# Performance work log

Hardware: AMD Instinct MI355X
Metric: run time of the kernel (lower is better)

Reference implementation:

```python
import jax, jax.numpy as jnp
import numpy as np

C = 256      # channels
G = 8        # groups
K = 9        # 3x3 sampling points (DCNv4 default kernel_size=3)
DWK = 3      # dw_kernel_size (wrapper passes kernel_size=3)
OFFSET_SCALE = 1.0
N, H, W = 8, 64, 64


def setup_inputs() -> dict:
    key = jax.random.key(0)
    ks = jax.random.split(key, 6)
    def init(k, shape, fan):
        return jax.random.normal(k, shape, jnp.float32) * (fan ** -0.5)
    return {
        "x": jax.random.normal(ks[0], (N, C, H, W), jnp.float32),
        "dw_w": init(ks[1], (C, 1, DWK, DWK), DWK * DWK),   # depthwise conv (OIHW, groups=C)
        "dw_b": jnp.zeros((C,), jnp.float32),
        "om_w": init(ks[2], (G * K * 3, C), C) * 0.01,       # offset/mask linear (small offsets)
        "om_b": jnp.zeros((G * K * 3,), jnp.float32),
        "vp_w": init(ks[3], (C, C), C),                      # value_proj
        "vp_b": jnp.zeros((C,), jnp.float32),
        "op_w": init(ks[4], (C, C), C),                      # output_proj (output_bias=False)
    }


def reference(x, dw_w, dw_b, om_w, om_b, vp_w, vp_b, op_w):
    n, c, h, w = x.shape
    cg = c // G
    L = h * w
    # b c h w -> b (h w) c
    xf = x.transpose(0, 2, 3, 1).reshape(n, L, c)
    value = (xf @ vp_w.T + vp_b).reshape(n, L, G, cg)
    # offset/mask branch: depthwise conv on raw input, then linear
    om_in = jax.lax.conv_general_dilated(
        x, dw_w, (1, 1), "SAME", feature_group_count=c,
        dimension_numbers=("NCHW", "OIHW", "NCHW")) + dw_b[None, :, None, None]
    om = om_in.transpose(0, 2, 3, 1).reshape(n, L, c) @ om_w.T + om_b  # (n, L, G*K*3)
    om = om.reshape(n, h, w, G, K * 3)
    off = om[..., : 2 * K].reshape(n, h, w, G, K, 2) * OFFSET_SCALE     # (dy, dx) per point
    mask = om[..., 2 * K:]                                              # (n,h,w,G,K) raw (DCNv4: no softmax)
    # base 3x3 dilation-1 grid centered at each pixel
    d = jnp.arange(-1, 2, dtype=jnp.float32)
    dy, dx = jnp.meshgrid(d, d, indexing="ij")
    base = jnp.stack([dy.ravel(), dx.ravel()], -1)  # (K, 2)
    py = (jnp.arange(h, dtype=jnp.float32).reshape(1, h, 1, 1, 1)
          + base[:, 0].reshape(1, 1, 1, 1, K) + off[..., 0])  # (n,h,w,G,K)
    px = (jnp.arange(w, dtype=jnp.float32).reshape(1, 1, w, 1, 1)
          + base[:, 1].reshape(1, 1, 1, 1, K) + off[..., 1])
    y0 = jnp.floor(py); x0 = jnp.floor(px)
    ty = py - y0; tx = px - x0
    y0i = y0.astype(jnp.int32); x0i = x0.astype(jnp.int32)

    def gather(yi, xi, wgt):
        valid = (yi >= 0) & (yi < h) & (xi >= 0) & (xi < w)
        idx = jnp.clip(yi, 0, h - 1) * w + jnp.clip(xi, 0, w - 1)       # (n,h,w,G,K)
        idx = idx.transpose(0, 1, 2, 4, 3).reshape(n, L * K, G)[..., None]
        g = jnp.take_along_axis(value, idx, axis=1)                     # (n, L*K, G, cg)
        g = g.reshape(n, h, w, K, G, cg).transpose(0, 1, 2, 4, 3, 5)    # (n,h,w,G,K,cg)
        return g * (wgt * valid)[..., None]

    sampled = (gather(y0i,     x0i,     (1 - ty) * (1 - tx))
             + gather(y0i,     x0i + 1, (1 - ty) * tx)
             + gather(y0i + 1, x0i,     ty * (1 - tx))
             + gather(y0i + 1, x0i + 1, ty * tx))
    out = jnp.einsum("nhwgk,nhwgkc->nhwgc", mask, sampled)  # mask-weighted aggregation
    out = out.reshape(n, L, c) @ op_w.T                      # output_proj (no bias)
    # b (h w) c -> b c h w
    return out.reshape(n, h, w, c).transpose(0, 3, 1, 2)
```

## Files before the change

### kernel.cpp

```cpp
#include <hip/hip_runtime.h>
#include <math.h>

#define N_  8
#define C_  256
#define G_  8
#define CG_ 32
#define K_  9
#define H_  64
#define W_  64
#define L_  (H_*W_)
#define OM_ 216
#define OMP_ 256

using frag_ab = __attribute__((ext_vector_type(8))) short;
using frag_cd = __attribute__((ext_vector_type(4))) float;

__device__ __forceinline__ unsigned short f2bf(float f) {
    unsigned int u = __float_as_uint(f);
    u += 0x7FFFu + ((u >> 16) & 1u);
    return (unsigned short)(u >> 16);
}
__device__ __forceinline__ float bflo(unsigned int u) { return __uint_as_float(u << 16); }
__device__ __forceinline__ float bfhi(unsigned int u) { return __uint_as_float(u & 0xFFFF0000u); }

__device__ __forceinline__ void gld16(const void* g, void* l) {
    __builtin_amdgcn_global_load_lds((const __attribute__((address_space(1))) void*)g,
                                     (__attribute__((address_space(3))) void*)l, 16, 0, 0);
}

__global__ __launch_bounds__(256) void prep_kernel(const float* __restrict__ x,
                                                   const float* __restrict__ w,
                                                   const float* __restrict__ b,
                                                   const float* __restrict__ vp_w,
                                                   const float* __restrict__ om_w,
                                                   const float* __restrict__ om_b,
                                                   const float* __restrict__ op_w,
                                                   unsigned short* __restrict__ xb,
                                                   unsigned short* __restrict__ omb,
                                                   unsigned short* __restrict__ vp_wb,
                                                   unsigned short* __restrict__ om_wb,
                                                   float* __restrict__ om_bp,
                                                   unsigned short* __restrict__ op_wb) {
    const int n = blockIdx.z, y = blockIdx.y, c0 = blockIdx.x * 32;
    const int tid = threadIdx.x;
    __shared__ float xs[3][32][66];
    __shared__ __align__(16) unsigned short os[2][64][40];
    if (tid < 192) {
        int r = tid / 64, c = (tid / 2) % 32, e = tid & 1;
        xs[r][c][e * 65] = 0.f;
    }
    const float* xbase = x + ((size_t)n * C_ + c0) * L_;
    for (int i = tid; i < 3 * 32 * 16; i += 256) {
        int r = i >> 9, rem = i & 511, c = rem >> 4, x4 = (rem & 15) * 4;
        int yy = y + r - 1;
        float4 v = make_float4(0.f, 0.f, 0.f, 0.f);
        if ((unsigned)yy < (unsigned)H_) v = *(const float4*)(xbase + (size_t)c * L_ + yy * W_ + x4);
        xs[r][c][1 + x4] = v.x; xs[r][c][2 + x4] = v.y;
        xs[r][c][3 + x4] = v.z; xs[r][c][4 + x4] = v.w;
    }
    __syncthreads();

    const int c = tid & 31, x0 = (tid >> 5) * 8;
    float wv[9];
#pragma unroll
    for (int i = 0; i < 9; i++) wv[i] = w[(c0 + c) * 9 + i];
    const float bias = b[c0 + c];
    float o[8];
#pragma unroll
    for (int j = 0; j < 8; j++) o[j] = bias;
#pragma unroll
    for (int r = 0; r < 3; r++) {
        float v[10];
#pragma unroll
        for (int d = 0; d < 10; d++) v[d] = xs[r][c][x0 + d];
#pragma unroll
        for (int j = 0; j < 8; j++)
            o[j] += wv[r * 3] * v[j] + wv[r * 3 + 1] * v[j + 1] + wv[r * 3 + 2] * v[j + 2];
    }
#pragma unroll
    for (int j = 0; j < 8; j++) {
        os[0][x0 + j][c] = f2bf(xs[1][c][1 + x0 + j]);
        os[1][x0 + j][c] = f2bf(o[j]);
    }
    __syncthreads();

    const int l = tid >> 2, c8 = (tid & 3) * 8;
    uint4 va = *(const uint4*)&os[0][l][c8];
    uint4 vc = *(const uint4*)&os[1][l][c8];
    size_t dst = ((size_t)n * L_ + y * W_ + l) * C_ + c0 + c8;
    *(uint4*)(xb + dst) = va;
    *(uint4*)(omb + dst) = vc;

    if (n == 0) {
        int idx = (blockIdx.x + 8 * blockIdx.y) * 256 + tid;
        if (idx < C_ * C_) {
            vp_wb[idx] = f2bf(vp_w[idx]);
            op_wb[idx] = f2bf(op_w[idx]);
            om_wb[idx] = (idx < OM_ * C_) ? f2bf(om_w[idx]) : (unsigned short)0;
        }
        if (idx < OMP_) om_bp[idx] = (idx < OM_) ? om_b[idx] : 0.f;
    }
}

__global__ __launch_bounds__(256) void gemm12_kernel(const unsigned short* __restrict__ xb,
                                                     const unsigned short* __restrict__ omb,
                                                     const unsigned short* __restrict__ vp_wb,
                                                     const unsigned short* __restrict__ om_wb,
                                                     const float* __restrict__ vp_b,
                                                     const float* __restrict__ om_bp,
                                                     unsigned short* __restrict__ valueb,
                                                     float* __restrict__ omf) {
    __shared__ unsigned short As[128 * 32];
    __shared__ unsigned short Bs[128 * 32];
    const int which = blockIdx.z;
    const unsigned short* A = which ? omb : xb;
    const unsigned short* B = which ? om_wb : vp_wb;
    const float* bias = which ? om_bp : vp_b;
    const int tid = threadIdx.x;
    const long i0 = (long)blockIdx.x * 128;
    const long j0 = (long)blockIdx.y * 128;
    const unsigned short* Ab = A + i0 * C_;
    const unsigned short* Bb = B + j0 * C_;
    const int wave = tid >> 6, lane = tid & 63;
    const int iw = (wave & 1) * 64, jw = (wave >> 1) * 64;
    const int lm = lane & 15, kq = lane >> 4;
    const int srow = tid >> 2, scol = (tid & 3) * 8;

    frag_cd acc[4][4];
#pragma unroll
    for (int a = 0; a < 4; a++)
#pragma unroll
        for (int c = 0; c < 4; c++) acc[a][c] = (frag_cd){0.f, 0.f, 0.f, 0.f};

    for (int k0 = 0; k0 < C_; k0 += 32) {
        const unsigned short* ga0 = Ab + (long)srow * C_ + k0 + scol;
        const unsigned short* gb0 = Bb + (long)srow * C_ + k0 + scol;
        gld16(ga0,            As + tid * 8);
        gld16(ga0 + 64 * C_,  As + 2048 + tid * 8);
        gld16(gb0,            Bs + tid * 8);
        gld16(gb0 + 64 * C_,  Bs + 2048 + tid * 8);
        __syncthreads();
        frag_ab af[4], bfr[4];
#pragma unroll
        for (int mi = 0; mi < 4; mi++)
            af[mi] = *(const frag_ab*)&As[(iw + mi * 16 + lm) * 32 + kq * 8];
#pragma unroll
        for (int ni = 0; ni < 4; ni++)
            bfr[ni] = *(const frag_ab*)&Bs[(jw + ni * 16 + lm) * 32 + kq * 8];
#pragma unroll
        for (int mi = 0; mi < 4; mi++)
#pragma unroll
            for (int ni = 0; ni < 4; ni++)
                acc[mi][ni] = __builtin_amdgcn_mfma_f32_16x16x32_bf16(af[mi], bfr[ni], acc[mi][ni], 0, 0, 0);
        __syncthreads();
    }

    float bv[4];
#pragma unroll
    for (int ni = 0; ni < 4; ni++)
        bv[ni] = bias[(int)(j0 + jw + ni * 16 + lm)];

    const long ibase = i0 + iw + kq * 4;
    const long jbase = j0 + jw + lm;
#pragma unroll
    for (int mi = 0; mi < 4; mi++) {
#pragma unroll
        for (int ni = 0; ni < 4; ni++) {
            long j = jbase + ni * 16;
#pragma unroll
            for (int r = 0; r < 4; r++) {
                long i = ibase + mi * 16 + r;
                float v = acc[mi][ni][r] + bv[ni];
                if (which)
                    omf[i * OMP_ + j] = v;
                else
                    valueb[i * C_ + j] = f2bf(v);
            }
        }
    }
}

__global__ __launch_bounds__(256) void gemm3_kernel(const unsigned short* __restrict__ A,
                                                    const unsigned short* __restrict__ B,
                                                    float* __restrict__ Dv) {
    __shared__ unsigned short As[128 * 32];
    __shared__ unsigned short Bs[128 * 32];
    const int tid = threadIdx.x;
    const long i0 = (long)blockIdx.x * 128;
    const long j0 = (long)blockIdx.y * 128;
    const unsigned short* Ab = A + i0 * C_;
    const unsigned short* Bb = B + (long)blockIdx.z * L_ * C_ + j0 * C_;
    const int wave = tid >> 6, lane = tid & 63;
    const int iw = (wave & 1) * 64, jw = (wave >> 1) * 64;
    const int lm = lane & 15, kq = lane >> 4;
    const int srow = tid >> 2, scol = (tid & 3) * 8;

    frag_cd acc[4][4];
#pragma unroll
    for (int a = 0; a < 4; a++)
#pragma unroll
        for (int c = 0; c < 4; c++) acc[a][c] = (frag_cd){0.f, 0.f, 0.f, 0.f};

    for (int k0 = 0; k0 < C_; k0 += 32) {
        const unsigned short* ga0 = Ab + (long)srow * C_ + k0 + scol;
        const unsigned short* gb0 = Bb + (long)srow * C_ + k0 + scol;
        gld16(ga0,            As + tid * 8);
        gld16(ga0 + 64 * C_,  As + 2048 + tid * 8);
        gld16(gb0,            Bs + tid * 8);
        gld16(gb0 + 64 * C_,  Bs + 2048 + tid * 8);
        __syncthreads();
        frag_ab af[4], bfr[4];
#pragma unroll
        for (int mi = 0; mi < 4; mi++)
            af[mi] = *(const frag_ab*)&As[(iw + mi * 16 + lm) * 32 + kq * 8];
#pragma unroll
        for (int ni = 0; ni < 4; ni++)
            bfr[ni] = *(const frag_ab*)&Bs[(jw + ni * 16 + lm) * 32 + kq * 8];
#pragma unroll
        for (int mi = 0; mi < 4; mi++)
#pragma unroll
            for (int ni = 0; ni < 4; ni++)
                acc[mi][ni] = __builtin_amdgcn_mfma_f32_16x16x32_bf16(af[mi], bfr[ni], acc[mi][ni], 0, 0, 0);
        __syncthreads();
    }

    float* Db = Dv + (long)blockIdx.z * C_ * L_;
    const long ibase = i0 + iw + kq * 4;
    const long jbase = j0 + jw + lm;
#pragma unroll
    for (int mi = 0; mi < 4; mi++) {
#pragma unroll
        for (int ni = 0; ni < 4; ni++) {
            long j = jbase + ni * 16;
#pragma unroll
            for (int r = 0; r < 4; r++) {
                long i = ibase + mi * 16 + r;
                Db[i * L_ + j] = acc[mi][ni][r];
            }
        }
    }
}

__global__ __launch_bounds__(256) void sample_kernel(const unsigned short* __restrict__ value,
                                                     const float* __restrict__ om,
                                                     unsigned short* __restrict__ interm) {
    const int n = blockIdx.y;
    const int l0 = blockIdx.x * 8;
    const int tid = threadIdx.x;

    __shared__ float sOm[8 * OM_];
    __shared__ float4 wgt[64][9];
    __shared__ uint4  soff[64][9];

    const float* omsrc = om + ((size_t)n * L_ + l0) * OMP_;
    for (int i = tid; i < 8 * OM_; i += 256) {
        int pp = i / OM_;
        sOm[i] = omsrc[pp * OMP_ + (i - pp * OM_)];
    }
    __syncthreads();

    for (int it = tid; it < 576; it += 256) {
        int pair = it / 9, k = it - pair * 9;
        int p = pair >> 3, g = pair & 7;
        int l = l0 + p, y = l >> 6, xp2 = l & 63;
        const float* so = &sOm[p * OM_ + g * 27];
        float offy = so[2 * k], offx = so[2 * k + 1], mk = so[18 + k];
        float py = (float)(y + k / 3 - 1) + offy;
        float px = (float)(xp2 + k % 3 - 1) + offx;
        float fy = floorf(py), fx = floorf(px);
        float ty = py - fy, tx = px - fx;
        int y0 = (int)fy, x0i = (int)fx;
        int y1 = y0 + 1, x1 = x0i + 1;
        float vy0 = ((unsigned)y0 < (unsigned)H_) ? 1.f : 0.f;
        float vy1 = ((unsigned)y1 < (unsigned)H_) ? 1.f : 0.f;
        float vx0 = ((unsigned)x0i < (unsigned)W_) ? 1.f : 0.f;
        float vx1 = ((unsigned)x1 < (unsigned)W_) ? 1.f : 0.f;
        int cy0 = min(max(y0, 0), H_ - 1), cy1 = min(max(y1, 0), H_ - 1);
        int cx0 = min(max(x0i, 0), W_ - 1), cx1 = min(max(x1, 0), W_ - 1);
        wgt[pair][k] = make_float4(mk * (1.f - ty) * (1.f - tx) * vy0 * vx0,
                                   mk * (1.f - ty) * tx         * vy0 * vx1,
                                   mk * ty         * (1.f - tx) * vy1 * vx0,
                                   mk * ty         * tx         * vy1 * vx1);
        soff[pair][k] = make_uint4((unsigned)((cy0 * W_ + cx0) << 9),
                                   (unsigned)((cy0 * W_ + cx1) << 9),
                                   (unsigned)((cy1 * W_ + cx0) << 9),
                                   (unsigned)((cy1 * W_ + cx1) << 9));
    }
    __syncthreads();

    const int pair = tid >> 2, p = pair >> 3, g = pair & 7, c8 = (tid & 3) * 8;
    const char* vb = (const char*)(value + (size_t)n * L_ * C_ + g * CG_ + c8);
    float acc[8] = {0.f, 0.f, 0.f, 0.f, 0.f, 0.f, 0.f, 0.f};
#pragma unroll
    for (int k = 0; k < K_; k++) {
        float4 wk = wgt[pair][k];
        uint4  ok = soff[pair][k];
        const uint4 v00 = *(const uint4*)(vb + ok.x);
        const uint4 v01 = *(const uint4*)(vb + ok.y);
        const uint4 v10 = *(const uint4*)(vb + ok.z);
        const uint4 v11 = *(const uint4*)(vb + ok.w);
#define ACC8(V, WW) { \
        acc[0] += WW * bflo(V.x); acc[1] += WW * bfhi(V.x); \
        acc[2] += WW * bflo(V.y); acc[3] += WW * bfhi(V.y); \
        acc[4] += WW * bflo(V.z); acc[5] += WW * bfhi(V.z); \
        acc[6] += WW * bflo(V.w); acc[7] += WW * bfhi(V.w); }
        ACC8(v00, wk.x) ACC8(v01, wk.y) ACC8(v10, wk.z) ACC8(v11, wk.w)
#undef ACC8
    }
    uint4 pk;
    unsigned short* pp2 = (unsigned short*)&pk;
#pragma unroll
    for (int i = 0; i < 8; i++) pp2[i] = f2bf(acc[i]);
    *(uint4*)(interm + ((size_t)n * L_ + l0 + p) * C_ + g * CG_ + c8) = pk;
}

extern "C" void kernel_launch(void* const* d_in, const int* in_sizes, int n_in,
                              void* d_out, int out_size, void* d_ws, size_t ws_size,
                              hipStream_t stream) {
    const float* x    = (const float*)d_in[0];
    const float* dw_w = (const float*)d_in[1];
    const float* dw_b = (const float*)d_in[2];
    const float* om_w = (const float*)d_in[3];
    const float* om_b = (const float*)d_in[4];
    const float* vp_w = (const float*)d_in[5];
    const float* vp_b = (const float*)d_in[6];
    const float* op_w = (const float*)d_in[7];
    float* out = (float*)d_out;

    char* ws = (char*)d_ws;
    unsigned short* xb      = (unsigned short*)(ws);
    unsigned short* omb     = (unsigned short*)(ws + 16777216);
    unsigned short* valueb  = (unsigned short*)(ws + 33554432);
    float*          omf     = (float*)(ws + 50331648);
    unsigned short* vp_wb   = (unsigned short*)(ws + 83886080);
    unsigned short* om_wb   = (unsigned short*)(ws + 84017152);
    unsigned short* op_wb   = (unsigned short*)(ws + 84148224);
    float*          om_bp   = (float*)(ws + 84279296);
    unsigned short* intermb = xb;

    prep_kernel<<<dim3(C_ / 32, H_, N_), 256, 0, stream>>>(
        x, dw_w, dw_b, vp_w, om_w, om_b, op_w,
        xb, omb, vp_wb, om_wb, om_bp, op_wb);
    gemm12_kernel<<<dim3(256, 2, 2), 256, 0, stream>>>(
        xb, omb, vp_wb, om_wb, vp_b, om_bp, valueb, omf);
    sample_kernel<<<dim3(L_ / 8, N_), 256, 0, stream>>>(valueb, omf, intermb);
    gemm3_kernel<<<dim3(2, 32, N_), 256, 0, stream>>>(op_wb, intermb, out);
}
```

Before: 174.4 us.

## Fuse deformable sampling with output projection GEMM via shared-memory intermediate

Merges the sampling kernel and the output-projection GEMM into one kernel. Each block samples 64 pixels across all groups into an XOR-swizzled LDS tile, then runs MFMA against op_w read straight from global memory. This removes the global write and re-read of the bf16 intermediate and one kernel launch. In exchange the sampling runs as 8 serialized sub-steps with barriers, there are fewer blocks (512), and op_w is reloaded from global/L2 by every block.

Result: faster. 168.7 us (-3.2%).

```diff
diff --git a/kernel.cpp b/kernel.cpp
--- a/kernel.cpp
+++ b/kernel.cpp
@@ -180,138 +180,120 @@
     }
 }
 
-__global__ __launch_bounds__(256) void gemm3_kernel(const unsigned short* __restrict__ A,
-                                                    const unsigned short* __restrict__ B,
-                                                    float* __restrict__ Dv) {
-    __shared__ unsigned short As[128 * 32];
-    __shared__ unsigned short Bs[128 * 32];
+__global__ __launch_bounds__(256, 3) void samplegemm_kernel(const unsigned short* __restrict__ value,
+                                                            const float* __restrict__ om,
+                                                            const unsigned short* __restrict__ opw,
+                                                            float* __restrict__ out) {
+    const int n = blockIdx.y, l0 = blockIdx.x * 64;
     const int tid = threadIdx.x;
-    const long i0 = (long)blockIdx.x * 128;
-    const long j0 = (long)blockIdx.y * 128;
-    const unsigned short* Ab = A + i0 * C_;
-    const unsigned short* Bb = B + (long)blockIdx.z * L_ * C_ + j0 * C_;
-    const int wave = tid >> 6, lane = tid & 63;
-    const int iw = (wave & 1) * 64, jw = (wave >> 1) * 64;
-    const int lm = lane & 15, kq = lane >> 4;
-    const int srow = tid >> 2, scol = (tid & 3) * 8;
-
-    frag_cd acc[4][4];
-#pragma unroll
-    for (int a = 0; a < 4; a++)
-#pragma unroll
-        for (int c = 0; c < 4; c++) acc[a][c] = (frag_cd){0.f, 0.f, 0.f, 0.f};
-
-    for (int k0 = 0; k0 < C_; k0 += 32) {
-        const unsigned short* ga0 = Ab + (long)srow * C_ + k0 + scol;
-        const unsigned short* gb0 = Bb + (long)srow * C_ + k0 + scol;
-        gld16(ga0,            As + tid * 8);
-        gld16(ga0 + 64 * C_,  As + 2048 + tid * 8);
-        gld16(gb0,            Bs + tid * 8);
-        gld16(gb0 + 64 * C_,  Bs + 2048 + tid * 8);
-        __syncthreads();
-        frag_ab af[4], bfr[4];
-#pragma unroll
-        for (int mi = 0; mi < 4; mi++)
-            af[mi] = *(const frag_ab*)&As[(iw + mi * 16 + lm) * 32 + kq * 8];
-#pragma unroll
-        for (int ni = 0; ni < 4; ni++)
-            bfr[ni] = *(const frag_ab*)&Bs[(jw + ni * 16 + lm) * 32 + kq * 8];
-#pragma unroll
-        for (int mi = 0; mi < 4; mi++)
-#pragma unroll
-            for (int ni = 0; ni < 4; ni++)
-                acc[mi][ni] = __builtin_amdgcn_mfma_f32_16x16x32_bf16(af[mi], bfr[ni], acc[mi][ni], 0, 0, 0);
-        __syncthreads();
-    }
-
-    float* Db = Dv + (long)blockIdx.z * C_ * L_;
-    const long ibase = i0 + iw + kq * 4;
-    const long jbase = j0 + jw + lm;
-#pragma unroll
-    for (int mi = 0; mi < 4; mi++) {
-#pragma unroll
-        for (int ni = 0; ni < 4; ni++) {
-            long j = jbase + ni * 16;
-#pragma unroll
-            for (int r = 0; r < 4; r++) {
-                long i = ibase + mi * 16 + r;
-                Db[i * L_ + j] = acc[mi][ni][r];
-            }
-        }
-    }
-}
-
-__global__ __launch_bounds__(256) void sample_kernel(const unsigned short* __restrict__ value,
-                                                     const float* __restrict__ om,
-                                                     unsigned short* __restrict__ interm) {
-    const int n = blockIdx.y;
-    const int l0 = blockIdx.x * 8;
-    const int tid = threadIdx.x;
-
-    __shared__ float sOm[8 * OM_];
+    __shared__ __align__(16) unsigned short interm[64 * 256];
     __shared__ float4 wgt[64][9];
     __shared__ uint4  soff[64][9];
 
-    const float* omsrc = om + ((size_t)n * L_ + l0) * OMP_;
-    for (int i = tid; i < 8 * OM_; i += 256) {
-        int pp = i / OM_;
-        sOm[i] = omsrc[pp * OMP_ + (i - pp * OM_)];
+    const char* vbase = (const char*)(value + (size_t)n * L_ * C_);
+    const int lp = tid >> 2;
+    const int g = lp & 7;
+    const int c8i = tid & 3;
+    const int slot = tid & 31;
+    const char* vb = vbase + (size_t)(g * CG_ + c8i * 8) * 2;
+
+    for (int rep = 0; rep < 8; rep++) {
+        __syncthreads();
+        for (int it = tid; it < 576; it += 256) {
+            int pl = it / 9, k = it - pl * 9;
+            int p = rep * 8 + (pl >> 3), gg = pl & 7;
+            int l = l0 + p, y = l >> 6, xp2 = l & 63;
+            const float* so = om + ((size_t)n * L_ + l) * OMP_ + gg * 27;
+            float offy = so[2 * k], offx = so[2 * k + 1], mk = so[18 + k];
+            float py = (float)(y + k / 3 - 1) + offy;
+            float px = (float)(xp2 + k % 3 - 1) + offx;
+            float fy = floorf(py), fx = floorf(px);
+            float ty = py - fy, tx = px - fx;
+            int y0 = (int)fy, x0i = (int)fx;
+            int y1 = y0 + 1, x1 = x0i + 1;
+            float vy0 = ((unsigned)y0 < (unsigned)H_) ? 1.f : 0.f;
+            float vy1 = ((unsigned)y1 < (unsigned)H_) ? 1.f : 0.f;
+            float vx0 = ((unsigned)x0i < (unsigned)W_) ? 1.f : 0.f;
+            float vx1 = ((unsigned)x1 < (unsigned)W_) ? 1.f : 0.f;
+            int cy0 = min(max(y0, 0), H_ - 1), cy1 = min(max(y1, 0), H_ - 1);
+            int cx0 = min(max(x0i, 0), W_ - 1), cx1 = min(max(x1, 0), W_ - 1);
+            wgt[pl][k] = make_float4(mk * (1.f - ty) * (1.f - tx) * vy0 * vx0,
+                                     mk * (1.f - ty) * tx         * vy0 * vx1,
+                                     mk * ty         * (1.f - tx) * vy1 * vx0,
+                                     mk * ty         * tx         * vy1 * vx1);
+            soff[pl][k] = make_uint4((unsigned)((cy0 * W_ + cx0) << 9),
+                                     (unsigned)((cy0 * W_ + cx1) << 9),
+                                     (unsigned)((cy1 * W_ + cx0) << 9),
+                                     (unsigned)((cy1 * W_ + cx1) << 9));
+        }
+        __syncthreads();
+        const int p = rep * 8 + (lp >> 3);
+        float acc[8] = {0.f, 0.f, 0.f, 0.f, 0.f, 0.f, 0.f, 0.f};
+#pragma unroll
+        for (int k = 0; k < K_; k++) {
+            float4 wk = wgt[lp][k];
+            uint4  ok = soff[lp][k];
+            const uint4 v00 = *(const uint4*)(vb + ok.x);
+            const uint4 v01 = *(const uint4*)(vb + ok.y);
+            const uint4 v10 = *(const uint4*)(vb + ok.z);
+            const uint4 v11 = *(const uint4*)(vb + ok.w);
+#define ACC8(V, WW) { \
+            acc[0] += WW * bflo(V.x); acc[1] += WW * bfhi(V.x); \
+            acc[2] += WW * bflo(V.y); acc[3] += WW * bfhi(V.y); \
+            acc[4] += WW * bflo(V.z); acc[5] += WW * bfhi(V.z); \
+            acc[6] += WW * bflo(V.w); acc[7] += WW * bfhi(V.w); }
+            ACC8(v00, wk.x) ACC8(v01, wk.y) ACC8(v10, wk.z) ACC8(v11, wk.w)
+#undef ACC8
+        }
+        uint4 pk;
+        unsigned short* ps = (unsigned short*)&pk;
+#pragma unroll
+        for (int i = 0; i < 8; i++) ps[i] = f2bf(acc[i]);
+        int phys = slot ^ (p & 7);
+        *(uint4*)&interm[p * 256 + phys * 8] = pk;
     }
     __syncthreads();
 
-    for (int it = tid; it < 576; it += 256) {
-        int pair = it / 9, k = it - pair * 9;
-        int p = pair >> 3, g = pair & 7;
-        int l = l0 + p, y = l >> 6, xp2 = l & 63;
-        const float* so = &sOm[p * OM_ + g * 27];
-        float offy = so[2 * k], offx = so[2 * k + 1], mk = so[18 + k];
-        float py = (float)(y + k / 3 - 1) + offy;
-        float px = (float)(xp2 + k % 3 - 1) + offx;
-        float fy = floorf(py), fx = floorf(px);
-        float ty = py - fy, tx = px - fx;
-        int y0 = (int)fy, x0i = (int)fx;
-        int y1 = y0 + 1, x1 = x0i + 1;
-        float vy0 = ((unsigned)y0 < (unsigned)H_) ? 1.f : 0.f;
-        float vy1 = ((unsigned)y1 < (unsigned)H_) ? 1.f : 0.f;
-        float vx0 = ((unsigned)x0i < (unsigned)W_) ? 1.f : 0.f;
-        float vx1 = ((unsigned)x1 < (unsigned)W_) ? 1.f : 0.f;
-        int cy0 = min(max(y0, 0), H_ - 1), cy1 = min(max(y1, 0), H_ - 1);
-        int cx0 = min(max(x0i, 0), W_ - 1), cx1 = min(max(x1, 0), W_ - 1);
-        wgt[pair][k] = make_float4(mk * (1.f - ty) * (1.f - tx) * vy0 * vx0,
-                                   mk * (1.f - ty) * tx         * vy0 * vx1,
-                                   mk * ty         * (1.f - tx) * vy1 * vx0,
-                                   mk * ty         * tx         * vy1 * vx1);
-        soff[pair][k] = make_uint4((unsigned)((cy0 * W_ + cx0) << 9),
-                                   (unsigned)((cy0 * W_ + cx1) << 9),
-                                   (unsigned)((cy1 * W_ + cx0) << 9),
-                                   (unsigned)((cy1 * W_ + cx1) << 9));
-    }
-    __syncthreads();
-
-    const int pair = tid >> 2, p = pair >> 3, g = pair & 7, c8 = (tid & 3) * 8;
-    const char* vb = (const char*)(value + (size_t)n * L_ * C_ + g * CG_ + c8);
-    float acc[8] = {0.f, 0.f, 0.f, 0.f, 0.f, 0.f, 0.f, 0.f};
-#pragma unroll
-    for (int k = 0; k < K_; k++) {
-        float4 wk = wgt[pair][k];
-        uint4  ok = soff[pair][k];
-        const uint4 v00 = *(const uint4*)(vb + ok.x);
-        const uint4 v01 = *(const uint4*)(vb + ok.y);
-        const uint4 v10 = *(const uint4*)(vb + ok.z);
-        const uint4 v11 = *(const uint4*)(vb + ok.w);
-#define ACC8(V, WW) { \
-        acc[0] += WW * bflo(V.x); acc[1] += WW * bfhi(V.x); \
-        acc[2] += WW * bflo(V.y); acc[3] += WW * bfhi(V.y); \
-        acc[4] += WW * bflo(V.z); acc[5] += WW * bfhi(V.z); \
-        acc[6] += WW * bflo(V.w); acc[7] += WW * bfhi(V.w); }
-        ACC8(v00, wk.x) ACC8(v01, wk.y) ACC8(v10, wk.z) ACC8(v11, wk.w)
-#undef ACC8
-    }
-    uint4 pk;
-    unsigned short* pp2 = (unsigned short*)&pk;
-#pragma unroll
-    for (int i = 0; i < 8; i++) pp2[i] = f2bf(acc[i]);
-    *(uint4*)(interm + ((size_t)n * L_ + l0 + p) * C_ + g * CG_ + c8) = pk;
+    const int wave = tid >> 6, lane = tid & 63;
+    const int lm = lane & 15, kq = lane >> 4;
+    const int q0w = wave * 64;
+    frag_cd acc2[4][4];
+#pragma unroll
+    for (int a = 0; a < 4; a++)
+#pragma unroll
+        for (int c = 0; c < 4; c++) acc2[a][c] = (frag_cd){0.f, 0.f, 0.f, 0.f};
+
+    for (int k0 = 0; k0 < C_; k0 += 32) {
+        frag_ab af[4], bfr[4];
+#pragma unroll
+        for (int mi = 0; mi < 4; mi++)
+            af[mi] = *(const frag_ab*)(opw + (size_t)(q0w + mi * 16 + lm) * C_ + k0 + kq * 8);
+#pragma unroll
+        for (int ni = 0; ni < 4; ni++) {
+            int pxr = ni * 16 + lm;
+            int phys = (k0 / 8 + kq) ^ (pxr & 7);
+            bfr[ni] = *(const frag_ab*)&interm[pxr * 256 + phys * 8];
+        }
+#pragma unroll
+        for (int mi = 0; mi < 4; mi++)
+#pragma unroll
+            for (int ni = 0; ni < 4; ni++)
+                acc2[mi][ni] = __builtin_amdgcn_mfma_f32_16x16x32_bf16(af[mi], bfr[ni], acc2[mi][ni], 0, 0, 0);
+    }
+
+    float* ob = out + (size_t)n * C_ * L_ + l0;
+#pragma unroll
+    for (int mi = 0; mi < 4; mi++) {
+#pragma unroll
+        for (int ni = 0; ni < 4; ni++) {
+            int pxr = ni * 16 + lm;
+#pragma unroll
+            for (int r = 0; r < 4; r++) {
+                int q = q0w + mi * 16 + kq * 4 + r;
+                ob[(size_t)q * L_ + pxr] = acc2[mi][ni][r];
+            }
+        }
+    }
 }
 
 extern "C" void kernel_launch(void* const* d_in, const int* in_sizes, int n_in,
@@ -336,13 +318,11 @@
     unsigned short* om_wb   = (unsigned short*)(ws + 84017152);
     unsigned short* op_wb   = (unsigned short*)(ws + 84148224);
     float*          om_bp   = (float*)(ws + 84279296);
-    unsigned short* intermb = xb;
 
     prep_kernel<<<dim3(C_ / 32, H_, N_), 256, 0, stream>>>(
         x, dw_w, dw_b, vp_w, om_w, om_b, op_w,
         xb, omb, vp_wb, om_wb, om_bp, op_wb);
     gemm12_kernel<<<dim3(256, 2, 2), 256, 0, stream>>>(
         xb, omb, vp_wb, om_wb, vp_b, om_bp, valueb, omf);
-    sample_kernel<<<dim3(L_ / 8, N_), 256, 0, stream>>>(valueb, omf, intermb);
-    gemm3_kernel<<<dim3(2, 32, N_), 256, 0, stream>>>(op_wb, intermb, out);
-}
+    samplegemm_kernel<<<dim3(L_ / 64, N_), 256, 0, stream>>>(valueb, omf, op_wb, out);
+}
```

## Stage value row bands in LDS for deformable sampling per group

Applied to the files above, without the earlier changes.

Replaces the sampling kernel with one that gives each block a single group and an 8-row band. The block preloads a 12-row halo of value channels for that group into shared memory and serves the bilinear taps from LDS, falling back to global loads only when a tap lands outside the staged rows. Offsets are packed into one 32-bit word per tap. The aim is to cut scattered global gathers through reuse in LDS, at the cost of fewer blocks (512 instead of 4096), about 48KB of LDS per block, and a serial loop over 8 rows with barriers.

After: 188.0 us. +7.8%, slower.

```diff
diff --git a/kernel.cpp b/kernel.cpp
--- a/kernel.cpp
+++ b/kernel.cpp
@@ -180,6 +180,101 @@
     }
 }
 
+__global__ __launch_bounds__(256, 2) void sample_lds_kernel(const unsigned short* __restrict__ value,
+                                                            const float* __restrict__ om,
+                                                            unsigned short* __restrict__ interm) {
+    const int n = blockIdx.y;
+    const int bx = blockIdx.x;
+    const int g = bx & 7;
+    const int band = bx >> 3;
+    const int y0 = band * 8;
+    const int tid = threadIdx.x;
+
+    __shared__ __align__(16) char vstage[4 * 12304];
+    __shared__ float4 wgt[64][9];
+    __shared__ unsigned soffp[64][9];
+
+    {
+        const int w = tid >> 6, lane = tid & 63;
+        const char* gsrc = (const char*)value +
+            ((size_t)n * L_ * C_ + (size_t)lane * C_ + g * CG_ + w * 8) * 2;
+        char* ldst = vstage + w * 12304 + lane * 16;
+#pragma unroll
+        for (int r = 0; r < 12; r++) {
+            int srow = min(max(y0 - 2 + r, 0), H_ - 1);
+            gld16(gsrc + (size_t)srow * (W_ * C_ * 2), ldst + r * 1024);
+        }
+    }
+
+    const int lp = tid >> 2;
+    const int c8i = tid & 3;
+    const char* vsb = vstage + c8i * 12304;
+    const char* vbg = (const char*)value + ((size_t)n * L_ * C_ + g * CG_ + c8i * 8) * 2;
+
+    for (int p = 0; p < 8; p++) {
+        __syncthreads();
+        const int row = y0 + p;
+        for (int it = tid; it < 576; it += 256) {
+            int px = it / 9, k = it - px * 9;
+            const float* so = om + ((size_t)n * L_ + row * W_ + px) * OMP_ + g * 27;
+            float offy = so[2 * k], offx = so[2 * k + 1], mk = so[18 + k];
+            float py = (float)(row + k / 3 - 1) + offy;
+            float px2 = (float)(px + k % 3 - 1) + offx;
+            float fy = floorf(py), fx = floorf(px2);
+            float ty = py - fy, tx = px2 - fx;
+            int iy0 = (int)fy, ix0 = (int)fx;
+            int iy1 = iy0 + 1, ix1 = ix0 + 1;
+            float vy0 = ((unsigned)iy0 < (unsigned)H_) ? 1.f : 0.f;
+            float vy1 = ((unsigned)iy1 < (unsigned)H_) ? 1.f : 0.f;
+            float vx0 = ((unsigned)ix0 < (unsigned)W_) ? 1.f : 0.f;
+            float vx1 = ((unsigned)ix1 < (unsigned)W_) ? 1.f : 0.f;
+            int cy0 = min(max(iy0, 0), H_ - 1), cy1 = min(max(iy1, 0), H_ - 1);
+            int cx0 = min(max(ix0, 0), W_ - 1), cx1 = min(max(ix1, 0), W_ - 1);
+            wgt[px][k] = make_float4(mk * (1.f - ty) * (1.f - tx) * vy0 * vx0,
+                                     mk * (1.f - ty) * tx         * vy0 * vx1,
+                                     mk * ty         * (1.f - tx) * vy1 * vx0,
+                                     mk * ty         * tx         * vy1 * vx1);
+            soffp[px][k] = (unsigned)cy0 | ((unsigned)cy1 << 8) |
+                           ((unsigned)cx0 << 16) | ((unsigned)cx1 << 24);
+        }
+        __syncthreads();
+        float acc[8] = {0.f, 0.f, 0.f, 0.f, 0.f, 0.f, 0.f, 0.f};
+#pragma unroll
+        for (int k = 0; k < K_; k++) {
+            float4 wk = wgt[lp][k];
+            unsigned cc = soffp[lp][k];
+            int cy0 = cc & 255, cy1 = (cc >> 8) & 255;
+            int cx0 = (cc >> 16) & 255, cx1 = (cc >> 24) & 255;
+            int s0 = cy0 - y0 + 2, s1 = cy1 - y0 + 2;
+            int cs0 = min(max(s0, 0), 11), cs1 = min(max(s1, 0), 11);
+            uint4 v00 = *(const uint4*)(vsb + cs0 * 1024 + cx0 * 16);
+            uint4 v01 = *(const uint4*)(vsb + cs0 * 1024 + cx1 * 16);
+            uint4 v10 = *(const uint4*)(vsb + cs1 * 1024 + cx0 * 16);
+            uint4 v11 = *(const uint4*)(vsb + cs1 * 1024 + cx1 * 16);
+            if ((unsigned)s0 >= 12u) {
+                v00 = *(const uint4*)(vbg + (size_t)((cy0 << 6) + cx0) * 512);
+                v01 = *(const uint4*)(vbg + (size_t)((cy0 << 6) + cx1) * 512);
+            }
+            if ((unsigned)s1 >= 12u) {
+                v10 = *(const uint4*)(vbg + (size_t)((cy1 << 6) + cx0) * 512);
+                v11 = *(const uint4*)(vbg + (size_t)((cy1 << 6) + cx1) * 512);
+            }
+#define ACC8(V, WW) { \
+            acc[0] += WW * bflo(V.x); acc[1] += WW * bfhi(V.x); \
+            acc[2] += WW * bflo(V.y); acc[3] += WW * bfhi(V.y); \
+            acc[4] += WW * bflo(V.z); acc[5] += WW * bfhi(V.z); \
+            acc[6] += WW * bflo(V.w); acc[7] += WW * bfhi(V.w); }
+            ACC8(v00, wk.x) ACC8(v01, wk.y) ACC8(v10, wk.z) ACC8(v11, wk.w)
+#undef ACC8
+        }
+        uint4 pk;
+        unsigned short* ps = (unsigned short*)&pk;
+#pragma unroll
+        for (int i = 0; i < 8; i++) ps[i] = f2bf(acc[i]);
+        *(uint4*)(interm + ((size_t)n * L_ + row * W_ + lp) * C_ + g * CG_ + c8i * 8) = pk;
+    }
+}
+
 __global__ __launch_bounds__(256) void gemm3_kernel(const unsigned short* __restrict__ A,
                                                     const unsigned short* __restrict__ B,
                                                     float* __restrict__ Dv) {
@@ -241,79 +336,6 @@
     }
 }
 
-__global__ __launch_bounds__(256) void sample_kernel(const unsigned short* __restrict__ value,
-                                                     const float* __restrict__ om,
-                                                     unsigned short* __restrict__ interm) {
-    const int n = blockIdx.y;
-    const int l0 = blockIdx.x * 8;
-    const int tid = threadIdx.x;
-
-    __shared__ float sOm[8 * OM_];
-    __shared__ float4 wgt[64][9];
-    __shared__ uint4  soff[64][9];
-
-    const float* omsrc = om + ((size_t)n * L_ + l0) * OMP_;
-    for (int i = tid; i < 8 * OM_; i += 256) {
-        int pp = i / OM_;
-        sOm[i] = omsrc[pp * OMP_ + (i - pp * OM_)];
-    }
-    __syncthreads();
-
-    for (int it = tid; it < 576; it += 256) {
-        int pair = it / 9, k = it - pair * 9;
-        int p = pair >> 3, g = pair & 7;
-        int l = l0 + p, y = l >> 6, xp2 = l & 63;
-        const float* so = &sOm[p * OM_ + g * 27];
-        float offy = so[2 * k], offx = so[2 * k + 1], mk = so[18 + k];
-        float py = (float)(y + k / 3 - 1) + offy;
-        float px = (float)(xp2 + k % 3 - 1) + offx;
-        float fy = floorf(py), fx = floorf(px);
-        float ty = py - fy, tx = px - fx;
-        int y0 = (int)fy, x0i = (int)fx;
-        int y1 = y0 + 1, x1 = x0i + 1;
-        float vy0 = ((unsigned)y0 < (unsigned)H_) ? 1.f : 0.f;
-        float vy1 = ((unsigned)y1 < (unsigned)H_) ? 1.f : 0.f;
-        float vx0 = ((unsigned)x0i < (unsigned)W_) ? 1.f : 0.f;
-        float vx1 = ((unsigned)x1 < (unsigned)W_) ? 1.f : 0.f;
-        int cy0 = min(max(y0, 0), H_ - 1), cy1 = min(max(y1, 0), H_ - 1);
-        int cx0 = min(max(x0i, 0), W_ - 1), cx1 = min(max(x1, 0), W_ - 1);
-        wgt[pair][k] = make_float4(mk * (1.f - ty) * (1.f - tx) * vy0 * vx0,
-                                   mk * (1.f - ty) * tx         * vy0 * vx1,
-                                   mk * ty         * (1.f - tx) * vy1 * vx0,
-                                   mk * ty         * tx         * vy1 * vx1);
-        soff[pair][k] = make_uint4((unsigned)((cy0 * W_ + cx0) << 9),
-                                   (unsigned)((cy0 * W_ + cx1) << 9),
-                                   (unsigned)((cy1 * W_ + cx0) << 9),
-                                   (unsigned)((cy1 * W_ + cx1) << 9));
-    }
-    __syncthreads();
-
-    const int pair = tid >> 2, p = pair >> 3, g = pair & 7, c8 = (tid & 3) * 8;
-    const char* vb = (const char*)(value + (size_t)n * L_ * C_ + g * CG_ + c8);
-    float acc[8] = {0.f, 0.f, 0.f, 0.f, 0.f, 0.f, 0.f, 0.f};
-#pragma unroll
-    for (int k = 0; k < K_; k++) {
-        float4 wk = wgt[pair][k];
-        uint4  ok = soff[pair][k];
-        const uint4 v00 = *(const uint4*)(vb + ok.x);
-        const uint4 v01 = *(const uint4*)(vb + ok.y);
-        const uint4 v10 = *(const uint4*)(vb + ok.z);
-        const uint4 v11 = *(const uint4*)(vb + ok.w);
-#define ACC8(V, WW) { \
-        acc[0] += WW * bflo(V.x); acc[1] += WW * bfhi(V.x); \
-        acc[2] += WW * bflo(V.y); acc[3] += WW * bfhi(V.y); \
-        acc[4] += WW * bflo(V.z); acc[5] += WW * bfhi(V.z); \
-        acc[6] += WW * bflo(V.w); acc[7] += WW * bfhi(V.w); }
-        ACC8(v00, wk.x) ACC8(v01, wk.y) ACC8(v10, wk.z) ACC8(v11, wk.w)
-#undef ACC8
-    }
-    uint4 pk;
-    unsigned short* pp2 = (unsigned short*)&pk;
-#pragma unroll
-    for (int i = 0; i < 8; i++) pp2[i] = f2bf(acc[i]);
-    *(uint4*)(interm + ((size_t)n * L_ + l0 + p) * C_ + g * CG_ + c8) = pk;
-}
-
 extern "C" void kernel_launch(void* const* d_in, const int* in_sizes, int n_in,
                               void* d_out, int out_size, void* d_ws, size_t ws_size,
                               hipStream_t stream) {
@@ -343,6 +365,6 @@
         xb, omb, vp_wb, om_wb, om_bp, op_wb);
     gemm12_kernel<<<dim3(256, 2, 2), 256, 0, stream>>>(
         xb, omb, vp_wb, om_wb, vp_b, om_bp, valueb, omf);
-    sample_kernel<<<dim3(L_ / 8, N_), 256, 0, stream>>>(valueb, omf, intermb);
+    sample_lds_kernel<<<dim3(64, N_), 256, 0, stream>>>(valueb, omf, intermb);
     gemm3_kernel<<<dim3(2, 32, N_), 256, 0, stream>>>(op_wb, intermb, out);
 }
```

## Prefetch next bilinear taps, swizzle block order, drop om staging in sampler

Applied to the files above, without the earlier changes.

The sampling kernel drops the shared-memory staging pass for the offset/mask row and reads offsets directly from global memory in the weight-computation loop. The gather loop is software-pipelined so the four value loads for the next kernel point are issued before the current point is accumulated. Block indices are remapped with an interleave (bx&7)<<6 | bx>>3, and launch bounds now request 4 blocks per CU. Together these aim to hide gather latency and raise occupancy, at the cost of more live registers and less coalesced om reads.

Result: faster. 170.1 us (-2.4%).

```diff
diff --git a/kernel.cpp b/kernel.cpp
--- a/kernel.cpp
+++ b/kernel.cpp
@@ -180,6 +180,81 @@
     }
 }
 
+__global__ __launch_bounds__(256, 4) void sample_kernel(const unsigned short* __restrict__ value,
+                                                        const float* __restrict__ om,
+                                                        unsigned short* __restrict__ interm) {
+    const int n = blockIdx.y;
+    const int bx = blockIdx.x;
+    const int t = ((bx & 7) << 6) + (bx >> 3);
+    const int l0 = t * 8;
+    const int tid = threadIdx.x;
+
+    __shared__ float4 wgt[64][9];
+    __shared__ uint4  soff[64][9];
+
+    for (int it = tid; it < 576; it += 256) {
+        int pl = it / 9, k = it - pl * 9;
+        int p = pl >> 3, g = pl & 7;
+        int l = l0 + p, y = l >> 6, xp2 = l & 63;
+        const float* so = om + ((size_t)n * L_ + l) * OMP_ + g * 27;
+        float offy = so[2 * k], offx = so[2 * k + 1], mk = so[18 + k];
+        float py = (float)(y + k / 3 - 1) + offy;
+        float px = (float)(xp2 + k % 3 - 1) + offx;
+        float fy = floorf(py), fx = floorf(px);
+        float ty = py - fy, tx = px - fx;
+        int y0 = (int)fy, x0i = (int)fx;
+        int y1 = y0 + 1, x1 = x0i + 1;
+        float vy0 = ((unsigned)y0 < (unsigned)H_) ? 1.f : 0.f;
+        float vy1 = ((unsigned)y1 < (unsigned)H_) ? 1.f : 0.f;
+        float vx0 = ((unsigned)x0i < (unsigned)W_) ? 1.f : 0.f;
+        float vx1 = ((unsigned)x1 < (unsigned)W_) ? 1.f : 0.f;
+        int cy0 = min(max(y0, 0), H_ - 1), cy1 = min(max(y1, 0), H_ - 1);
+        int cx0 = min(max(x0i, 0), W_ - 1), cx1 = min(max(x1, 0), W_ - 1);
+        wgt[pl][k] = make_float4(mk * (1.f - ty) * (1.f - tx) * vy0 * vx0,
+                                 mk * (1.f - ty) * tx         * vy0 * vx1,
+                                 mk * ty         * (1.f - tx) * vy1 * vx0,
+                                 mk * ty         * tx         * vy1 * vx1);
+        soff[pl][k] = make_uint4((unsigned)((cy0 * W_ + cx0) << 9),
+                                 (unsigned)((cy0 * W_ + cx1) << 9),
+                                 (unsigned)((cy1 * W_ + cx0) << 9),
+                                 (unsigned)((cy1 * W_ + cx1) << 9));
+    }
+    __syncthreads();
+
+    const int lp = tid >> 2, p = lp >> 3, g = lp & 7, c8 = (tid & 3) * 8;
+    const char* vb = (const char*)(value + (size_t)n * L_ * C_ + g * CG_ + c8);
+    float acc[8] = {0.f, 0.f, 0.f, 0.f, 0.f, 0.f, 0.f, 0.f};
+    uint4  ok = soff[lp][0];
+    float4 wk = wgt[lp][0];
+    uint4 v00 = *(const uint4*)(vb + ok.x);
+    uint4 v01 = *(const uint4*)(vb + ok.y);
+    uint4 v10 = *(const uint4*)(vb + ok.z);
+    uint4 v11 = *(const uint4*)(vb + ok.w);
+#pragma unroll
+    for (int k = 0; k < K_; k++) {
+        const int kn = (k < K_ - 1) ? k + 1 : k;
+        uint4  ok2 = soff[lp][kn];
+        float4 wk2 = wgt[lp][kn];
+        uint4 n00 = *(const uint4*)(vb + ok2.x);
+        uint4 n01 = *(const uint4*)(vb + ok2.y);
+        uint4 n10 = *(const uint4*)(vb + ok2.z);
+        uint4 n11 = *(const uint4*)(vb + ok2.w);
+#define ACC8(V, WW) { \
+        acc[0] += WW * bflo(V.x); acc[1] += WW * bfhi(V.x); \
+        acc[2] += WW * bflo(V.y); acc[3] += WW * bfhi(V.y); \
+        acc[4] += WW * bflo(V.z); acc[5] += WW * bfhi(V.z); \
+        acc[6] += WW * bflo(V.w); acc[7] += WW * bfhi(V.w); }
+        ACC8(v00, wk.x) ACC8(v01, wk.y) ACC8(v10, wk.z) ACC8(v11, wk.w)
+#undef ACC8
+        v00 = n00; v01 = n01; v10 = n10; v11 = n11; wk = wk2;
+    }
+    uint4 pk;
+    unsigned short* ps = (unsigned short*)&pk;
+#pragma unroll
+    for (int i = 0; i < 8; i++) ps[i] = f2bf(acc[i]);
+    *(uint4*)(interm + ((size_t)n * L_ + l0 + p) * C_ + g * CG_ + c8) = pk;
+}
+
 __global__ __launch_bounds__(256) void gemm3_kernel(const unsigned short* __restrict__ A,
                                                     const unsigned short* __restrict__ B,
                                                     float* __restrict__ Dv) {
@@ -241,79 +316,6 @@
     }
 }
 
-__global__ __launch_bounds__(256) void sample_kernel(const unsigned short* __restrict__ value,
-                                                     const float* __restrict__ om,
-                                                     unsigned short* __restrict__ interm) {
-    const int n = blockIdx.y;
-    const int l0 = blockIdx.x * 8;
-    const int tid = threadIdx.x;
-
-    __shared__ float sOm[8 * OM_];
-    __shared__ float4 wgt[64][9];
-    __shared__ uint4  soff[64][9];
-
-    const float* omsrc = om + ((size_t)n * L_ + l0) * OMP_;
-    for (int i = tid; i < 8 * OM_; i += 256) {
-        int pp = i / OM_;
-        sOm[i] = omsrc[pp * OMP_ + (i - pp * OM_)];
-    }
-    __syncthreads();
-
-    for (int it = tid; it < 576; it += 256) {
-        int pair = it / 9, k = it - pair * 9;
-        int p = pair >> 3, g = pair & 7;
-        int l = l0 + p, y = l >> 6, xp2 = l & 63;
-        const float* so = &sOm[p * OM_ + g * 27];
-        float offy = so[2 * k], offx = so[2 * k + 1], mk = so[18 + k];
-        float py = (float)(y + k / 3 - 1) + offy;
-        float px = (float)(xp2 + k % 3 - 1) + offx;
-        float fy = floorf(py), fx = floorf(px);
-        float ty = py - fy, tx = px - fx;
-        int y0 = (int)fy, x0i = (int)fx;
-        int y1 = y0 + 1, x1 = x0i + 1;
-        float vy0 = ((unsigned)y0 < (unsigned)H_) ? 1.f : 0.f;
-        float vy1 = ((unsigned)y1 < (unsigned)H_) ? 1.f : 0.f;
-        float vx0 = ((unsigned)x0i < (unsigned)W_) ? 1.f : 0.f;
-        float vx1 = ((unsigned)x1 < (unsigned)W_) ? 1.f : 0.f;
-        int cy0 = min(max(y0, 0), H_ - 1), cy1 = min(max(y1, 0), H_ - 1);
-        int cx0 = min(max(x0i, 0), W_ - 1), cx1 = min(max(x1, 0), W_ - 1);
-        wgt[pair][k] = make_float4(mk * (1.f - ty) * (1.f - tx) * vy0 * vx0,
-                                   mk * (1.f - ty) * tx         * vy0 * vx1,
-                                   mk * ty         * (1.f - tx) * vy1 * vx0,
-                                   mk * ty         * tx         * vy1 * vx1);
-        soff[pair][k] = make_uint4((unsigned)((cy0 * W_ + cx0) << 9),
-                                   (unsigned)((cy0 * W_ + cx1) << 9),
-                                   (unsigned)((cy1 * W_ + cx0) << 9),
-                                   (unsigned)((cy1 * W_ + cx1) << 9));
-    }
-    __syncthreads();
-
-    const int pair = tid >> 2, p = pair >> 3, g = pair & 7, c8 = (tid & 3) * 8;
-    const char* vb = (const char*)(value + (size_t)n * L_ * C_ + g * CG_ + c8);
-    float acc[8] = {0.f, 0.f, 0.f, 0.f, 0.f, 0.f, 0.f, 0.f};
-#pragma unroll
-    for (int k = 0; k < K_; k++) {
-        float4 wk = wgt[pair][k];
-        uint4  ok = soff[pair][k];
-        const uint4 v00 = *(const uint4*)(vb + ok.x);
-        const uint4 v01 = *(const uint4*)(vb + ok.y);
-        const uint4 v10 = *(const uint4*)(vb + ok.z);
-        const uint4 v11 = *(const uint4*)(vb + ok.w);
-#define ACC8(V, WW) { \
-        acc[0] += WW * bflo(V.x); acc[1] += WW * bfhi(V.x); \
-        acc[2] += WW * bflo(V.y); acc[3] += WW * bfhi(V.y); \
-        acc[4] += WW * bflo(V.z); acc[5] += WW * bfhi(V.z); \
-        acc[6] += WW * bflo(V.w); acc[7] += WW * bfhi(V.w); }
-        ACC8(v00, wk.x) ACC8(v01, wk.y) ACC8(v10, wk.z) ACC8(v11, wk.w)
-#undef ACC8
-    }
-    uint4 pk;
-    unsigned short* pp2 = (unsigned short*)&pk;
-#pragma unroll
-    for (int i = 0; i < 8; i++) pp2[i] = f2bf(acc[i]);
-    *(uint4*)(interm + ((size_t)n * L_ + l0 + p) * C_ + g * CG_ + c8) = pk;
-}
-
 extern "C" void kernel_launch(void* const* d_in, const int* in_sizes, int n_in,
                               void* d_out, int out_size, void* d_ws, size_t ws_size,
                               hipStream_t stream) {
@@ -343,6 +345,6 @@
         xb, omb, vp_wb, om_wb, om_bp, op_wb);
     gemm12_kernel<<<dim3(256, 2, 2), 256, 0, stream>>>(
         xb, omb, vp_wb, om_wb, vp_b, om_bp, valueb, omf);
-    sample_kernel<<<dim3(L_ / 8, N_), 256, 0, stream>>>(valueb, omf, intermb);
+    sample_kernel<<<dim3(512, N_), 256, 0, stream>>>(valueb, omf, intermb);
     gemm3_kernel<<<dim3(2, 32, N_), 256, 0, stream>>>(op_wb, intermb, out);
 }
```
